# Kernel optimization log

Hardware: AMD Instinct MI355X
Metric: run time of the kernel (lower is better)

## Reference

```python
import jax, jax.numpy as jnp
import numpy as np

B, N, NC = 16, 25200, 80
CONF_THRES = 0.25
IOU_THRES = 0.45
MAX_DET = 300
MAX_WH = 7680.0   # yolov5 per-class box offset for class-aware NMS
TOPK = 1024       # pre-NMS candidate cap (fixed-shape stand-in for yolov5 max_nms)


def setup_inputs():
    key = jax.random.key(0)
    k1, k2 = jax.random.split(key)
    # xywh in pixel units (640x640 image, boxes up to ~120 px); obj/cls confidences in [0,1]
    xywh = jax.random.uniform(k1, (B, N, 4), dtype=jnp.float32) * jnp.array([640.0, 640.0, 120.0, 120.0], jnp.float32)
    conf = jax.random.uniform(k2, (B, N, 1 + NC), dtype=jnp.float32)
    return {"YOLOoutput": jnp.concatenate([xywh, conf], axis=-1)}


def _xywh2xyxy(x):
    cx, cy, w, h = x[..., 0], x[..., 1], x[..., 2], x[..., 3]
    return jnp.stack([cx - w / 2, cy - h / 2, cx + w / 2, cy + h / 2], axis=-1)


def _pairwise_iou(a, b):
    # a, b: [K,4] xyxy -> [K,K]
    lt = jnp.maximum(a[:, None, :2], b[None, :, :2])
    rb = jnp.minimum(a[:, None, 2:], b[None, :, 2:])
    wh = jnp.maximum(rb - lt, 0.0)
    inter = wh[..., 0] * wh[..., 1]
    area_a = (a[:, 2] - a[:, 0]) * (a[:, 3] - a[:, 1])
    area_b = (b[:, 2] - b[:, 0]) * (b[:, 3] - b[:, 1])
    return inter / (area_a[:, None] + area_b[None, :] - inter + 1e-7)


def _nms_single(pred):
    # pred: [N, 5+NC]
    obj = pred[:, 4]
    cls_conf = pred[:, 5:] * obj[:, None]      # conf = obj_conf * cls_conf (yolov5)
    conf = jnp.max(cls_conf, axis=-1)
    j = jnp.argmax(cls_conf, axis=-1)
    valid = (obj > CONF_THRES) & (conf > CONF_THRES)
    box = _xywh2xyxy(pred[:, :4])
    scores = jnp.where(valid, conf, -1.0)      # invalid candidates sink to bottom
    top_scores, idx = jax.lax.top_k(scores, TOPK)
    b = box[idx]                               # [TOPK,4]
    c = j[idx].astype(box.dtype)
    boxes_off = b + (c * MAX_WH)[:, None]      # class-aware NMS via per-class offset
    valid_k = top_scores > 0.0
    iou = _pairwise_iou(boxes_off, boxes_off)
    ar = jnp.arange(TOPK)

    def body(i, supp):
        active = jnp.logical_not(supp[i])
        return supp | (active & (iou[i] > IOU_THRES) & (ar > i))

    supp = jax.lax.fori_loop(0, TOPK, body, jnp.logical_not(valid_k))
    keep = valid_k & jnp.logical_not(supp)
    fs, fi = jax.lax.top_k(jnp.where(keep, top_scores, -1.0), MAX_DET)
    dv = fs > 0.0
    det_box = b[fi] * dv[:, None]              # zero out padded rows
    det = jnp.concatenate(
        [det_box, jnp.where(dv, fs, 0.0)[:, None], (c[fi] * dv)[:, None]], axis=-1
    )                                          # [MAX_DET, 6] = x1,y1,x2,y2,conf,cls
    return det, dv


def reference(YOLOoutput):
    det, dvalid = jax.vmap(_nms_single)(YOLOoutput)   # [B,MAX_DET,6], [B,MAX_DET]
    scores = det[..., 4]
    mean_conf = jnp.max(scores, axis=1)               # = 0 when image has no detections
    n = dvalid.sum(axis=1)
    terms = jnp.abs(det[..., 0:2] - det[..., 2:4]) * scores[..., None]  # padded rows are 0
    s = terms.sum(axis=(1, 2))
    wh = jnp.where(n > 0, s / (2.0 * jnp.maximum(n, 1)), 0.0)  # mean over n*2 elements
    conf_addition = mean_conf.sum() / B
    w_and_h = wh.sum() / B
    return conf_addition, w_and_h, det[2]
```

## Files before the change

kernel.cpp:

```cpp
#include <hip/hip_runtime.h>
#include <hip/hip_bf16.h>

typedef unsigned long long u64;
typedef unsigned int u32;

#define BATCH 16
#define NANCH 25200
#define NCLS 80
#define NFEAT 85
#define TOPK 1024
#define MAXDET 300
#define CONF_T 0.25f
#define IOU_T 0.45f
#define MAX_WH 7680.0f

#define TILE_A 64
#define TILES_PER_BLK 2

__global__ __launch_bounds__(256) void score_kernel(const float* __restrict__ in,
                                                    u64* __restrict__ keys) {
    __shared__ float ld[TILE_A * NFEAT];
    const int b = blockIdx.y, tid = threadIdx.x;
    for (int t = 0; t < TILES_PER_BLK; ++t) {
        const int tile = blockIdx.x * TILES_PER_BLK + t;
        const int a0 = tile * TILE_A;
        if (a0 >= NANCH) break;
        const int na = min(TILE_A, NANCH - a0);
        const int nf4 = na * NFEAT / 4;
        const float4* src = (const float4*)(in + ((size_t)b * NANCH + a0) * NFEAT);
        if (t) __syncthreads();
        for (int k = tid; k < nf4; k += 256) ((float4*)ld)[k] = src[k];
        __syncthreads();
        const int a = tid >> 2, q = tid & 3;
        if (a < na) {
            const float* p = ld + a * NFEAT;
            float obj = p[4];
            float best = -1e30f;
            int bj = 0;
#pragma unroll
            for (int k = 0; k < 20; ++k) {
                float v = p[5 + q * 20 + k] * obj;
                if (v > best) { best = v; bj = q * 20 + k; }
            }
#pragma unroll
            for (int d = 1; d < 4; d <<= 1) {
                float ob = __shfl_xor(best, d, 64);
                int oj = __shfl_xor(bj, d, 64);
                if (ob > best || (ob == best && oj < bj)) { best = ob; bj = oj; }
            }
            if (q == 0) {
                bool valid = (obj > CONF_T) && (best > CONF_T);
                float sc = valid ? best : -1.0f;
                u32 sb = __float_as_uint(sc);
                u32 ord = sb ^ ((sb & 0x80000000u) ? 0xFFFFFFFFu : 0x80000000u);
                int idx = a0 + a;
                keys[(size_t)b * NANCH + idx] =
                    ((u64)ord << 32) | ((u64)((u32)(idx ^ 0xFFFF) & 0xFFFFu) << 8) | (u64)bj;
            }
        }
    }
}

__global__ __launch_bounds__(1024) void select_topk(const u64* __restrict__ keys,
                                                    const float* __restrict__ in,
                                                    float4* __restrict__ box4,
                                                    float4* __restrict__ boxoff4,
                                                    float* __restrict__ score,
                                                    float* __restrict__ cls,
                                                    u64* __restrict__ vmask) {
    const int b = blockIdx.x, tid = threadIdx.x;
    const int lane = tid & 63, wv = tid >> 6;
    const u64* kb = keys + (size_t)b * NANCH;
    __shared__ u32 hist[4096];
    __shared__ u32 wtot[16];
    __shared__ u32 wsfx[16];
    __shared__ u32 s_prefix12, s_cnt;
    __shared__ u64 buf[2048];

#pragma unroll
    for (int i = 0; i < 4; ++i) hist[tid * 4 + i] = 0u;
    __syncthreads();
#pragma unroll 4
    for (int n = tid; n < NANCH; n += 1024) {
        u32 hi = (u32)(kb[n] >> 32);
        atomicAdd(&hist[hi >> 20], 1u);
    }
    __syncthreads();
    u32 h0 = hist[tid * 4], h1 = hist[tid * 4 + 1];
    u32 h2 = hist[tid * 4 + 2], h3 = hist[tid * 4 + 3];
    u32 s3v = h3, s2v = h2 + s3v, s1v = h1 + s2v, s0v = h0 + s1v;
    u32 S = s0v;
#pragma unroll
    for (int d = 1; d < 64; d <<= 1) {
        u32 o = __shfl_down(S, d, 64);
        if (lane + d < 64) S += o;
    }
    if (lane == 0) wtot[wv] = S;
    __syncthreads();
    if (tid == 0) {
        u32 acc = 0;
        for (int w = 15; w >= 0; --w) { wsfx[w] = acc; acc += wtot[w]; }
    }
    __syncthreads();
    {
        const u32 E = wsfx[wv] + (S - s0v);
        const u32 v0 = E + s0v, v1 = E + s1v, v2 = E + s2v, v3 = E + s3v, v4 = E;
        if (v0 >= (u32)TOPK && v1 < (u32)TOPK) s_prefix12 = (u32)(tid * 4 + 0);
        if (v1 >= (u32)TOPK && v2 < (u32)TOPK) s_prefix12 = (u32)(tid * 4 + 1);
        if (v2 >= (u32)TOPK && v3 < (u32)TOPK) s_prefix12 = (u32)(tid * 4 + 2);
        if (v3 >= (u32)TOPK && v4 < (u32)TOPK) s_prefix12 = (u32)(tid * 4 + 3);
    }
    if (tid == 0) s_cnt = 0u;
    __syncthreads();
    const u32 p12 = s_prefix12;
#pragma unroll 4
    for (int n = tid; n < NANCH; n += 1024) {
        u64 k = kb[n];
        if (((u32)(k >> 32) >> 20) > p12) {
            u32 pos = atomicAdd(&s_cnt, 1u);
            if (pos < 2048u) buf[pos] = k;
        }
    }
    __syncthreads();
#pragma unroll 4
    for (int n = tid; n < NANCH; n += 1024) {
        u64 k = kb[n];
        if (((u32)(k >> 32) >> 20) == p12) {
            u32 pos = atomicAdd(&s_cnt, 1u);
            if (pos < 2048u) buf[pos] = k;
        }
    }
    __syncthreads();
    u32 cnt = s_cnt; if (cnt > 2048u) cnt = 2048u;
    for (int n = (int)cnt + tid; n < 2048; n += 1024) buf[n] = 0ull;
    __syncthreads();

    const int base = wv * 128;
    u64 r0 = buf[base + lane], r1 = buf[base + 64 + lane];
    for (int k2 = 2; k2 <= 128; k2 <<= 1) {
        const bool d0 = (((base + lane) & k2) == 0);
        const bool d1 = (((base + 64 + lane) & k2) == 0);
        for (int jj = (k2 >> 1); jj >= 1; jj >>= 1) {
            if (jj == 64) {
                u64 mx = r0 > r1 ? r0 : r1, mn = r0 > r1 ? r1 : r0;
                r0 = d0 ? mx : mn; r1 = d0 ? mn : mx;
            } else {
                const bool up = (lane & jj) != 0;
                u64 v0 = __shfl_xor(r0, jj, 64);
                u64 v1 = __shfl_xor(r1, jj, 64);
                const bool km0 = (d0 != up), km1 = (d1 != up);
                r0 = km0 ? (r0 > v0 ? r0 : v0) : (r0 < v0 ? r0 : v0);
                r1 = km1 ? (r1 > v1 ? r1 : v1) : (r1 < v1 ? r1 : v1);
            }
        }
    }
    for (int k2 = 256; k2 <= 2048; k2 <<= 1) {
        buf[base + lane] = r0; buf[base + 64 + lane] = r1;
        __syncthreads();
        for (int jj = (k2 >> 1); jj >= 128; jj >>= 1) {
            int i = ((tid & ~(jj - 1)) << 1) | (tid & (jj - 1));
            int part = i | jj;
            u64 a = buf[i], c = buf[part];
            bool sw = ((i & k2) == 0) ? (a < c) : (a > c);
            if (sw) { buf[i] = c; buf[part] = a; }
            __syncthreads();
        }
        r0 = buf[base + lane]; r1 = buf[base + 64 + lane];
        const bool d0 = (((base + lane) & k2) == 0);
        for (int jj = 64; jj >= 1; jj >>= 1) {
            if (jj == 64) {
                u64 mx = r0 > r1 ? r0 : r1, mn = r0 > r1 ? r1 : r0;
                r0 = d0 ? mx : mn; r1 = d0 ? mn : mx;
            } else {
                const bool up = (lane & jj) != 0;
                u64 v0 = __shfl_xor(r0, jj, 64);
                u64 v1 = __shfl_xor(r1, jj, 64);
                const bool km = (d0 != up);
                r0 = km ? (r0 > v0 ? r0 : v0) : (r0 < v0 ? r0 : v0);
                r1 = km ? (r1 > v1 ? r1 : v1) : (r1 < v1 ? r1 : v1);
            }
        }
    }
    buf[base + lane] = r0; buf[base + 64 + lane] = r1;
    __syncthreads();

    u64 k = buf[tid];
    u32 ord = (u32)(k >> 32);
    u32 sb = (ord & 0x80000000u) ? (ord ^ 0x80000000u) : ~ord;
    float sc = __uint_as_float(sb);
    int idx = (int)((((u32)(k >> 8)) & 0xFFFFu) ^ 0xFFFFu);
    int j = (int)(k & 0xFFu);
    const float* pr = in + ((size_t)b * NANCH + idx) * NFEAT;
    float cx = pr[0], cy = pr[1], ww = pr[2], hh = pr[3];
    float x1 = cx - ww / 2.0f, y1 = cy - hh / 2.0f;
    float x2 = cx + ww / 2.0f, y2 = cy + hh / 2.0f;
    float c = (float)j;
    float cm = c * MAX_WH;
    box4[b * TOPK + tid]    = make_float4(x1, y1, x2, y2);
    boxoff4[b * TOPK + tid] = make_float4(x1 + cm, y1 + cm, x2 + cm, y2 + cm);
    score[b * TOPK + tid] = sc;
    cls[b * TOPK + tid] = c;
    u64 bal = __ballot(sc > 0.0f);
    if ((tid & 63) == 0) vmask[b * 16 + (tid >> 6)] = bal;
}

__global__ __launch_bounds__(256) void iou_mask(const float4* __restrict__ boxoff4,
                                                u64* __restrict__ M) {
    const int wavei = (blockIdx.x << 2) | (threadIdx.x >> 6);
    const int lane = threadIdx.x & 63;
    const int b = wavei >> 10;
    const int i = wavei & 1023;
    const float4 A = boxoff4[b * TOPK + i];
    const float areaA = (A.z - A.x) * (A.w - A.y);
    u64 myword = 0ull;
#pragma unroll 4
    for (int t = 0; t < 16; ++t) {
        int j = (t << 6) | lane;
        float4 Bx = boxoff4[b * TOPK + j];
        float lx = fmaxf(A.x, Bx.x), ly = fmaxf(A.y, Bx.y);
        float rx = fminf(A.z, Bx.z), ry = fminf(A.w, Bx.w);
        float iw = fmaxf(rx - lx, 0.0f), ih = fmaxf(ry - ly, 0.0f);
        float inter = iw * ih;
        float areaB = (Bx.z - Bx.x) * (Bx.w - Bx.y);
        float iou = inter / (areaA + areaB - inter + 1e-7f);
        bool pred = (iou > IOU_T) && (j > i);
        u64 bal = __ballot(pred);
        if (lane == t) myword = bal;
    }
    if (lane < 16) M[((size_t)b * TOPK + i) * 16 + lane] = myword;
}

__global__ __launch_bounds__(64) void nms_finalize(const u64* __restrict__ M,
                                                   const u64* __restrict__ vmask,
                                                   const float4* __restrict__ box4,
                                                   const float* __restrict__ score,
                                                   const float* __restrict__ cls,
                                                   float* __restrict__ out) {
    const int b = blockIdx.x, lane = threadIdx.x;
    __shared__ u64 kw[16];
    __shared__ int wpfx[17];
    __shared__ float sdet[MAXDET * 6];
    __shared__ float s_sum, s_max;
    if (lane == 0) { s_sum = 0.0f; s_max = 0.0f; }
    if (lane < 16) {
        const int w = lane;
        const u64 vm = vmask[b * 16 + w];
        u64 supp = ~vm;
        const u64* Mb = M + (size_t)b * TOPK * 16;
        u64 rwA[16], rwB[16];
#pragma unroll
        for (int q = 0; q < 16; ++q) rwA[q] = Mb[q * 16 + w];
        for (int wb = 0; wb < 16; ++wb) {
            u64 cur = __shfl(supp, wb, 64);
#pragma unroll
            for (int c4 = 0; c4 < 4; ++c4) {
                const int rn = wb * 64 + (c4 + 1) * 16;
                if (rn < 1024) {
#pragma unroll
                    for (int q = 0; q < 16; ++q) rwB[q] = Mb[(rn + q) * 16 + w];
                }
                u64 rc[16];
#pragma unroll
                for (int q = 0; q < 16; ++q) rc[q] = __shfl(rwA[q], wb, 64);
#pragma unroll
                for (int q = 0; q < 16; ++q) {
                    const int ii = c4 * 16 + q;
                    const bool act = ((cur >> ii) & 1ull) == 0ull;
                    supp = act ? (supp | rwA[q]) : supp;
                    cur  = act ? (cur  | rc[q])  : cur;
                }
#pragma unroll
                for (int q = 0; q < 16; ++q) rwA[q] = rwB[q];
            }
        }
        kw[w] = vm & ~supp;
    }
    __syncthreads();
    if (lane == 0) {
        int acc = 0;
        for (int w = 0; w < 16; ++w) { wpfx[w] = acc; acc += __popcll(kw[w]); }
        wpfx[16] = acc;
    }
    for (int t = lane; t < MAXDET * 6; t += 64) sdet[t] = 0.0f;
    __syncthreads();
    for (int r = lane; r < TOPK; r += 64) {
        int w = r >> 6, bp = r & 63;
        if ((kw[w] >> bp) & 1ull) {
            int pos = wpfx[w] + __popcll(kw[w] & ((1ull << bp) - 1ull));
            if (pos < MAXDET) {
                float4 bx = box4[b * TOPK + r];
                float s = score[b * TOPK + r];
                float c = cls[b * TOPK + r];
                sdet[pos * 6 + 0] = bx.x;
                sdet[pos * 6 + 1] = bx.y;
                sdet[pos * 6 + 2] = bx.z;
                sdet[pos * 6 + 3] = bx.w;
                sdet[pos * 6 + 4] = s;
                sdet[pos * 6 + 5] = c;
                float term = (fabsf(bx.x - bx.z) + fabsf(bx.y - bx.w)) * s;
                atomicAdd(&s_sum, term);
                if (pos == 0) s_max = s;
            }
        }
    }
    __syncthreads();
    if (lane == 0) {
        int n = wpfx[16]; if (n > MAXDET) n = MAXDET;
        float wh = (n > 0) ? (s_sum / (2.0f * (float)n)) : 0.0f;
        atomicAdd(&out[0], s_max / (float)BATCH);
        atomicAdd(&out[1], wh / (float)BATCH);
    }
    if (b == 2) {
        for (int t = lane; t < MAXDET * 6; t += 64) out[2 + t] = sdet[t];
    }
}

extern "C" void kernel_launch(void* const* d_in, const int* in_sizes, int n_in,
                              void* d_out, int out_size, void* d_ws, size_t ws_size,
                              hipStream_t stream) {
    const float* in = (const float*)d_in[0];
    float* out = (float*)d_out;
    char* ws = (char*)d_ws;

    u64*    keys     = (u64*)   (ws + 0);
    float4* boxoff4  = (float4*)(ws + 3225600);
    float4* box4     = (float4*)(ws + 3487744);
    float*  score    = (float*) (ws + 3749888);
    float*  cls      = (float*) (ws + 3815424);
    u64*    vmask    = (u64*)   (ws + 3880960);
    u64*    M        = (u64*)   (ws + 3883008);

    hipMemsetAsync(out, 0, 2 * sizeof(float), stream);
    score_kernel<<<dim3(197, BATCH), 256, 0, stream>>>(in, keys);
    select_topk<<<BATCH, 1024, 0, stream>>>(keys, in, box4, boxoff4, score, cls, vmask);
    iou_mask<<<BATCH * TOPK / 4, 256, 0, stream>>>(boxoff4, M);
    nms_finalize<<<BATCH, 64, 0, stream>>>(M, vmask, box4, score, cls, out);
}
```

Baseline: 304.0 us.

## Use direct global-to-LDS loads, stage boxes and NMS mask in shared memory

The score kernel now processes one tile per block, with twice as many blocks, and fills LDS with global_load_lds 16-byte async copies instead of register round-trips. The IoU mask kernel first stages each image's 1024 offset boxes in shared memory, so the box loads no longer go to global memory. The NMS finalize kernel runs 512 threads, which bulk-copy the 128 KB suppression matrix into LDS before the serial 16-lane scan reads rows from LDS rather than from global memory. This trades larger LDS use and an extra copy phase for lower latency on the serial dependency chain.

Result: faster. 297.4 us (-2.2%).

```diff
diff --git a/kernel.cpp b/kernel.cpp
--- a/kernel.cpp
+++ b/kernel.cpp
@@ -15,48 +15,55 @@
 #define MAX_WH 7680.0f
 
 #define TILE_A 64
-#define TILES_PER_BLK 2
+
+__device__ __forceinline__ void gload_lds16(const void* g, void* l) {
+    __builtin_amdgcn_global_load_lds(
+        (const __attribute__((address_space(1))) unsigned int*)g,
+        (__attribute__((address_space(3))) unsigned int*)l, 16, 0, 0);
+}
 
 __global__ __launch_bounds__(256) void score_kernel(const float* __restrict__ in,
                                                     u64* __restrict__ keys) {
     __shared__ float ld[TILE_A * NFEAT];
     const int b = blockIdx.y, tid = threadIdx.x;
-    for (int t = 0; t < TILES_PER_BLK; ++t) {
-        const int tile = blockIdx.x * TILES_PER_BLK + t;
-        const int a0 = tile * TILE_A;
-        if (a0 >= NANCH) break;
-        const int na = min(TILE_A, NANCH - a0);
-        const int nf4 = na * NFEAT / 4;
-        const float4* src = (const float4*)(in + ((size_t)b * NANCH + a0) * NFEAT);
-        if (t) __syncthreads();
-        for (int k = tid; k < nf4; k += 256) ((float4*)ld)[k] = src[k];
-        __syncthreads();
-        const int a = tid >> 2, q = tid & 3;
-        if (a < na) {
-            const float* p = ld + a * NFEAT;
-            float obj = p[4];
-            float best = -1e30f;
-            int bj = 0;
-#pragma unroll
-            for (int k = 0; k < 20; ++k) {
-                float v = p[5 + q * 20 + k] * obj;
-                if (v > best) { best = v; bj = q * 20 + k; }
-            }
-#pragma unroll
-            for (int d = 1; d < 4; d <<= 1) {
-                float ob = __shfl_xor(best, d, 64);
-                int oj = __shfl_xor(bj, d, 64);
-                if (ob > best || (ob == best && oj < bj)) { best = ob; bj = oj; }
-            }
-            if (q == 0) {
-                bool valid = (obj > CONF_T) && (best > CONF_T);
-                float sc = valid ? best : -1.0f;
-                u32 sb = __float_as_uint(sc);
-                u32 ord = sb ^ ((sb & 0x80000000u) ? 0xFFFFFFFFu : 0x80000000u);
-                int idx = a0 + a;
-                keys[(size_t)b * NANCH + idx] =
-                    ((u64)ord << 32) | ((u64)((u32)(idx ^ 0xFFFF) & 0xFFFFu) << 8) | (u64)bj;
-            }
+    const int wv = tid >> 6, lane = tid & 63;
+    const int a0 = blockIdx.x * TILE_A;
+    const int na = min(TILE_A, NANCH - a0);
+    const int nbytes = na * NFEAT * 4;
+    const char* gbase = (const char*)(in + ((size_t)b * NANCH + a0) * NFEAT);
+#pragma unroll
+    for (int r = 0; r < 6; ++r) {
+        const int off = (r * 4 + wv) << 10;
+        const int myb = off + lane * 16;
+        if (myb < nbytes)
+            gload_lds16(gbase + myb, (char*)ld + off);
+    }
+    __syncthreads();
+    const int a = tid >> 2, q = tid & 3;
+    if (a < na) {
+        const float* p = ld + a * NFEAT;
+        float obj = p[4];
+        float best = -1e30f;
+        int bj = 0;
+#pragma unroll
+        for (int k = 0; k < 20; ++k) {
+            float v = p[5 + q * 20 + k] * obj;
+            if (v > best) { best = v; bj = q * 20 + k; }
+        }
+#pragma unroll
+        for (int d = 1; d < 4; d <<= 1) {
+            float ob = __shfl_xor(best, d, 64);
+            int oj = __shfl_xor(bj, d, 64);
+            if (ob > best || (ob == best && oj < bj)) { best = ob; bj = oj; }
+        }
+        if (q == 0) {
+            bool valid = (obj > CONF_T) && (best > CONF_T);
+            float sc = valid ? best : -1.0f;
+            u32 sb = __float_as_uint(sc);
+            u32 ord = sb ^ ((sb & 0x80000000u) ? 0xFFFFFFFFu : 0x80000000u);
+            int idx = a0 + a;
+            keys[(size_t)b * NANCH + idx] =
+                ((u64)ord << 32) | ((u64)((u32)(idx ^ 0xFFFF) & 0xFFFFu) << 8) | (u64)bj;
         }
     }
 }
@@ -206,17 +213,19 @@
 
 __global__ __launch_bounds__(256) void iou_mask(const float4* __restrict__ boxoff4,
                                                 u64* __restrict__ M) {
-    const int wavei = (blockIdx.x << 2) | (threadIdx.x >> 6);
+    __shared__ float4 sbx[TOPK];
+    const int b = blockIdx.x >> 8;
+    const int i = ((blockIdx.x & 255) << 2) | (threadIdx.x >> 6);
     const int lane = threadIdx.x & 63;
-    const int b = wavei >> 10;
-    const int i = wavei & 1023;
-    const float4 A = boxoff4[b * TOPK + i];
+    for (int t = threadIdx.x; t < TOPK; t += 256) sbx[t] = boxoff4[b * TOPK + t];
+    __syncthreads();
+    const float4 A = sbx[i];
     const float areaA = (A.z - A.x) * (A.w - A.y);
     u64 myword = 0ull;
 #pragma unroll 4
     for (int t = 0; t < 16; ++t) {
         int j = (t << 6) | lane;
-        float4 Bx = boxoff4[b * TOPK + j];
+        float4 Bx = sbx[j];
         float lx = fmaxf(A.x, Bx.x), ly = fmaxf(A.y, Bx.y);
         float rx = fminf(A.z, Bx.z), ry = fminf(A.w, Bx.w);
         float iw = fmaxf(rx - lx, 0.0f), ih = fmaxf(ry - ly, 0.0f);
@@ -230,26 +239,34 @@
     if (lane < 16) M[((size_t)b * TOPK + i) * 16 + lane] = myword;
 }
 
-__global__ __launch_bounds__(64) void nms_finalize(const u64* __restrict__ M,
-                                                   const u64* __restrict__ vmask,
-                                                   const float4* __restrict__ box4,
-                                                   const float* __restrict__ score,
-                                                   const float* __restrict__ cls,
-                                                   float* __restrict__ out) {
-    const int b = blockIdx.x, lane = threadIdx.x;
+__global__ __launch_bounds__(512) void nms_finalize(const u64* __restrict__ M,
+                                                    const u64* __restrict__ vmask,
+                                                    const float4* __restrict__ box4,
+                                                    const float* __restrict__ score,
+                                                    const float* __restrict__ cls,
+                                                    float* __restrict__ out) {
+    __shared__ u64 sM[TOPK * 16];
     __shared__ u64 kw[16];
     __shared__ int wpfx[17];
     __shared__ float sdet[MAXDET * 6];
     __shared__ float s_sum, s_max;
-    if (lane == 0) { s_sum = 0.0f; s_max = 0.0f; }
-    if (lane < 16) {
-        const int w = lane;
+    const int b = blockIdx.x, tid = threadIdx.x;
+    {
+        const ulonglong2* Ms = (const ulonglong2*)(M + (size_t)b * TOPK * 16);
+        ulonglong2* Ldst = (ulonglong2*)sM;
+#pragma unroll 4
+        for (int t = tid; t < TOPK * 8; t += 512) Ldst[t] = Ms[t];
+    }
+    for (int t = tid; t < MAXDET * 6; t += 512) sdet[t] = 0.0f;
+    if (tid == 0) { s_sum = 0.0f; s_max = 0.0f; }
+    __syncthreads();
+    if (tid < 16) {
+        const int w = tid;
         const u64 vm = vmask[b * 16 + w];
         u64 supp = ~vm;
-        const u64* Mb = M + (size_t)b * TOPK * 16;
         u64 rwA[16], rwB[16];
 #pragma unroll
-        for (int q = 0; q < 16; ++q) rwA[q] = Mb[q * 16 + w];
+        for (int q = 0; q < 16; ++q) rwA[q] = sM[q * 16 + w];
         for (int wb = 0; wb < 16; ++wb) {
             u64 cur = __shfl(supp, wb, 64);
 #pragma unroll
@@ -257,7 +274,7 @@
                 const int rn = wb * 64 + (c4 + 1) * 16;
                 if (rn < 1024) {
 #pragma unroll
-                    for (int q = 0; q < 16; ++q) rwB[q] = Mb[(rn + q) * 16 + w];
+                    for (int q = 0; q < 16; ++q) rwB[q] = sM[(rn + q) * 16 + w];
                 }
                 u64 rc[16];
 #pragma unroll
@@ -276,14 +293,13 @@
         kw[w] = vm & ~supp;
     }
     __syncthreads();
-    if (lane == 0) {
+    if (tid == 0) {
         int acc = 0;
         for (int w = 0; w < 16; ++w) { wpfx[w] = acc; acc += __popcll(kw[w]); }
         wpfx[16] = acc;
     }
-    for (int t = lane; t < MAXDET * 6; t += 64) sdet[t] = 0.0f;
-    __syncthreads();
-    for (int r = lane; r < TOPK; r += 64) {
+    __syncthreads();
+    for (int r = tid; r < TOPK; r += 512) {
         int w = r >> 6, bp = r & 63;
         if ((kw[w] >> bp) & 1ull) {
             int pos = wpfx[w] + __popcll(kw[w] & ((1ull << bp) - 1ull));
@@ -304,14 +320,14 @@
         }
     }
     __syncthreads();
-    if (lane == 0) {
+    if (tid == 0) {
         int n = wpfx[16]; if (n > MAXDET) n = MAXDET;
         float wh = (n > 0) ? (s_sum / (2.0f * (float)n)) : 0.0f;
         atomicAdd(&out[0], s_max / (float)BATCH);
         atomicAdd(&out[1], wh / (float)BATCH);
     }
     if (b == 2) {
-        for (int t = lane; t < MAXDET * 6; t += 64) out[2 + t] = sdet[t];
+        for (int t = tid; t < MAXDET * 6; t += 512) out[2 + t] = sdet[t];
     }
 }
 
@@ -331,8 +347,8 @@
     u64*    M        = (u64*)   (ws + 3883008);
 
     hipMemsetAsync(out, 0, 2 * sizeof(float), stream);
-    score_kernel<<<dim3(197, BATCH), 256, 0, stream>>>(in, keys);
+    score_kernel<<<dim3(394, BATCH), 256, 0, stream>>>(in, keys);
     select_topk<<<BATCH, 1024, 0, stream>>>(keys, in, box4, boxoff4, score, cls, vmask);
-    iou_mask<<<BATCH * TOPK / 4, 256, 0, stream>>>(boxoff4, M);
-    nms_finalize<<<BATCH, 64, 0, stream>>>(M, vmask, box4, score, cls, out);
-}
+    iou_mask<<<BATCH * 256, 256, 0, stream>>>(boxoff4, M);
+    nms_finalize<<<BATCH, 512, 0, stream>>>(M, vmask, box4, score, cls, out);
+}
```
